# Performance work log

Measured on AMD Instinct MI355X. Metric: run time of the kernel, lower is better.

Reference implementation:

```python
import jax, jax.numpy as jnp
import numpy as np

N_M, N_U = 50000, 100000          # movie / user node counts
D_IN, H, OUT = 128, 128, 64        # input feat, hidden_channels, out_channels
E_SIMS, E_REV = 800000, 1600000    # edge counts


def setup_inputs() -> dict:
    key = jax.random.key(0)
    ks = jax.random.split(key, 16)
    glorot = lambda k, i, o: jax.random.normal(k, (i, o), jnp.float32) * np.float32(1.0 / np.sqrt(i))
    return dict(
        x_movie=jax.random.normal(ks[0], (N_M, D_IN), jnp.float32),
        x_user=jax.random.normal(ks[1], (N_U, D_IN), jnp.float32),
        src_sims=jax.random.randint(ks[2], (E_SIMS,), 0, N_M, jnp.int32),
        dst_sims=jax.random.randint(ks[3], (E_SIMS,), 0, N_M, jnp.int32),
        src_rev=jax.random.randint(ks[4], (E_REV,), 0, N_M, jnp.int32),
        dst_rev=jax.random.randint(ks[5], (E_REV,), 0, N_U, jnp.int32),
        # SAGEConv params: lin_l (neighbor, with bias), lin_r (root, no bias)
        W1l=glorot(ks[6], D_IN, H), b1l=jnp.zeros((H,), jnp.float32), W1r=glorot(ks[7], D_IN, H),
        W2l=glorot(ks[8], D_IN, H), b2l=jnp.zeros((H,), jnp.float32), W2r=glorot(ks[9], D_IN, H),
        W3l=glorot(ks[10], H, H),   b3l=jnp.zeros((H,), jnp.float32), W3r=glorot(ks[11], H, H),
        # Post-conv dense layers
        Wl1=glorot(ks[12], H, H),  bl1=jnp.zeros((H,), jnp.float32),
        Wl2=glorot(ks[13], H, H),  bl2=jnp.zeros((H,), jnp.float32),
        Wl3=glorot(ks[14], H, OUT), bl3=jnp.zeros((OUT,), jnp.float32),
    )


def _sage(x_src, x_dst, src, dst, Wl, bl, Wr):
    """PyG SAGEConv (mean aggr): lin_l(mean_{j->i} x_src[j]) + lin_r(x_dst)."""
    n_dst = x_dst.shape[0]
    summ = jax.ops.segment_sum(x_src[src], dst, num_segments=n_dst)          # [n_dst, d]
    cnt = jax.ops.segment_sum(jnp.ones(src.shape, x_src.dtype), dst, num_segments=n_dst)
    mean = summ / jnp.maximum(cnt, 1.0)[:, None]                             # 0 for isolated nodes
    return mean @ Wl + bl + x_dst @ Wr


def reference(x_movie, x_user, src_sims, dst_sims, src_rev, dst_rev,
              W1l, b1l, W1r, W2l, b2l, W2r, W3l, b3l, W3r,
              Wl1, bl1, Wl2, bl2, Wl3, bl3):
    h = jax.nn.relu(_sage(x_movie, x_movie, src_sims, dst_sims, W1l, b1l, W1r))
    h = jax.nn.relu(h @ Wl1 + bl1)
    u = jax.nn.relu(_sage(x_movie, x_user, src_rev, dst_rev, W2l, b2l, W2r))
    u = jax.nn.relu(u @ Wl2 + bl2)
    u = jax.nn.relu(_sage(h, u, src_rev, dst_rev, W3l, b3l, W3r))
    return u @ Wl3 + bl3                                                     # [N_U, OUT]
```

## Files before the change

### kernel.cpp

```cpp
#include <hip/hip_runtime.h>


typedef float f32x4 __attribute__((ext_vector_type(4)));
typedef __bf16 bf16x8 __attribute__((ext_vector_type(8)));
typedef unsigned short us8 __attribute__((ext_vector_type(8)));
typedef unsigned long long ull;

#define CAP 64

struct BinInit { int off[16]; };

__device__ __forceinline__ unsigned short bf16_rne(float x) {
    unsigned u = __builtin_bit_cast(unsigned, x);
    unsigned r = (u + 0x7fffu + ((u >> 16) & 1u)) >> 16;
    return (unsigned short)r;
}
__device__ __forceinline__ float bf16_to_f(unsigned short b) {
    unsigned u = ((unsigned)b) << 16;
    return __builtin_bit_cast(float, u);
}
__device__ __forceinline__ void split_bf16(float x, unsigned short& h, unsigned short& l) {
    h = bf16_rne(x);
    l = bf16_rne(x - bf16_to_f(h));
}

__global__ __launch_bounds__(256) void prepconv_kernel(
    const float* __restrict__ W1l, const float* __restrict__ W1r,
    const float* __restrict__ W2l, const float* __restrict__ W2r,
    const float* __restrict__ W3l, const float* __restrict__ W3r,
    const float* __restrict__ Wl1, const float* __restrict__ Wl2,
    const float* __restrict__ Wl3,
    unsigned short* __restrict__ oh, unsigned short* __restrict__ ol,
    const float* __restrict__ xm, unsigned short* __restrict__ xmh,
    unsigned short* __restrict__ xml, unsigned short* __restrict__ itab,
    int n8, BinInit bi, int* __restrict__ binoff, int* __restrict__ bin_wcur)
{
    const int t = threadIdx.x;
    if (blockIdx.x == 0 && t < 16) {
        binoff[t] = bi.off[t];
        bin_wcur[t] = bi.off[t];
    }
    if (blockIdx.x < 544) {
        const int i = blockIdx.x * 256 + t;
        float v; int k, n, N, base;
        if (i < 98304) {
            const int s = i >> 15;
            const float* Wa = s == 0 ? W1l : (s == 1 ? W2l : W3l);
            const float* Wb = s == 0 ? W1r : (s == 1 ? W2r : W3r);
            base = s << 15; N = 128;
            const int local = i - base;
            k = local >> 7; n = local & 127;
            v = (k < 128) ? Wa[(size_t)k * 128 + n] : Wb[(size_t)(k - 128) * 128 + n];
        } else if (i < 131072) {
            const int s = (i - 98304) >> 14;
            const float* Wa = s ? Wl2 : Wl1;
            base = 98304 + (s << 14); N = 128;
            const int local = i - base;
            k = local >> 7; n = local & 127;
            v = Wa[(size_t)k * 128 + n];
        } else {
            base = 131072; N = 64;
            const int local = i - base;
            k = local >> 6; n = local & 63;
            v = Wl3[(size_t)k * 64 + n];
        }
        unsigned short h, l;
        split_bf16(v, h, l);
        const int ks = k >> 5, kg = (k >> 3) & 3, j = k & 7;
        const int slot = (n >> 4) * 64 + kg * 16 + (n & 15);
        const size_t pos = (size_t)base + ((size_t)ks * (N * 4) + slot) * 8 + j;
        oh[pos] = h;
        ol[pos] = l;
    } else {
        const int i = (blockIdx.x - 544) * 256 + t;
        if (i >= n8) return;
        us8 hv, lv;
#pragma unroll
        for (int j = 0; j < 8; ++j) {
            const float x = xm[(size_t)i * 8 + j];
            unsigned short h, l;
            split_bf16(x, h, l);
            hv[j] = h; lv[j] = l;
        }
        *(us8*)(xmh + (size_t)i * 8) = hv;
        *(us8*)(xml + (size_t)i * 8) = lv;
        const int r = i >> 4, c = (i & 15) * 8;
        *(us8*)(itab + (size_t)r * 256 + c) = hv;
    }
}

__global__ __launch_bounds__(256) void passA_kernel(
    const int* __restrict__ src_s, const int* __restrict__ dst_s,
    const int* __restrict__ src_r, const int* __restrict__ dst_r,
    int* __restrict__ bin_wcur, unsigned* __restrict__ pairs,
    int ES, int ER, int sm, int su)
{
    __shared__ int lcnt[16], loff[16], lbase[16];
    __shared__ ull stg[2048];
    const int t = threadIdx.x;
    const int total = ES + ER;
    const int base = blockIdx.x * 2048;
    if (t < 16) lcnt[t] = 0;
    __syncthreads();
    int mybin[8], myrank[8];
    ull mypack[8];
#pragma unroll
    for (int e = 0; e < 8; ++e) {
        const int i = base + e * 256 + t;
        mybin[e] = -1;
        if (i < total) {
            int s, d, b, local;
            if (i < ES) { s = src_s[i]; d = dst_s[i]; b = d >> sm; local = d & ((1 << sm) - 1); }
            else { s = src_r[i - ES]; d = dst_r[i - ES]; b = 8 + (d >> su); local = d & ((1 << su) - 1); }
            mybin[e] = b;
            mypack[e] = ((ull)b << 32) | ((unsigned)(local << 16) | (unsigned)s);
            myrank[e] = atomicAdd(&lcnt[b], 1);
        }
    }
    __syncthreads();
    if (t < 16) {
        const int v = lcnt[t];
        int incl = v;
#pragma unroll
        for (int off = 1; off < 16; off <<= 1) {
            const int y = __shfl_up(incl, off, 64);
            if (t >= off) incl += y;
        }
        loff[t] = incl - v;
        lbase[t] = atomicAdd(&bin_wcur[t], v);
    }
    __syncthreads();
#pragma unroll
    for (int e = 0; e < 8; ++e)
        if (mybin[e] >= 0) stg[loff[mybin[e]] + myrank[e]] = mypack[e];
    __syncthreads();
    const int cnt_total = loff[15] + lcnt[15];
    for (int i = t; i < cnt_total; i += 256) {
        const ull p = stg[i];
        const int b = (int)(p >> 32);
        pairs[lbase[b] + (i - loff[b])] = (unsigned)p;
    }
}

__global__ __launch_bounds__(256) void fillB_kernel(
    const unsigned* __restrict__ pairs, const int* __restrict__ binoff,
    const int* __restrict__ bin_wcur,
    int* __restrict__ cnt_m, int* __restrict__ cnt_u,
    int* __restrict__ srcs_s, int* __restrict__ srcs_r, int sm, int su)
{
    const int t = threadIdx.x;
    const int g = blockIdx.x & 7, bi = blockIdx.x >> 3, nb = gridDim.x >> 3;
#pragma unroll
    for (int which = 0; which < 2; ++which) {
        const int b = g + which * 8;
        const int beg = binoff[b], cnt = bin_wcur[b] - beg;
        const int dbase = which ? (g << su) : (g << sm);
        int* __restrict__ cn = which ? cnt_u : cnt_m;
        int* __restrict__ srcs = which ? srcs_r : srcs_s;
        for (int i = bi * 256 + t; i < cnt; i += nb * 256) {
            const unsigned p = pairs[beg + i];
            const int d = (int)(p >> 16) + dbase;
            const int pos = atomicAdd(&cn[d], 1);
            srcs[(size_t)d * CAP + pos] = (int)(p & 0xffffu);
        }
    }
}

__global__ __launch_bounds__(256) void gather_m_kernel(
    const unsigned short* __restrict__ it,
    const int* __restrict__ cnt, const int* __restrict__ srcs,
    unsigned short* __restrict__ o0h, unsigned short* __restrict__ o0l, int n_dst)
{
    const int wid = (blockIdx.x * 256 + threadIdx.x) >> 6;
    const int lane = threadIdx.x & 63;
    if (wid >= n_dst) return;
    const int nE = __builtin_amdgcn_readfirstlane(cnt[wid]);
    const int beg = wid * CAP;
    const int loff = lane * 2;
    float a0 = 0.f, a1 = 0.f;
    int e = 0;
    for (; e + 8 <= nE; e += 8) {
#pragma unroll
        for (int u = 0; u < 8; ++u) {
            const int s = srcs[beg + e + u];
            const unsigned v = *(const unsigned*)(it + (size_t)s * 256 + loff);
            a0 += __builtin_bit_cast(float, v << 16);
            a1 += __builtin_bit_cast(float, v & 0xffff0000u);
        }
    }
    for (; e < nE; ++e) {
        const int s = srcs[beg + e];
        const unsigned v = *(const unsigned*)(it + (size_t)s * 256 + loff);
        a0 += __builtin_bit_cast(float, v << 16);
        a1 += __builtin_bit_cast(float, v & 0xffff0000u);
    }
    const float inv = 1.0f / fmaxf((float)nE, 1.0f);
    unsigned short h0, l0, h1, l1;
    split_bf16(a0 * inv, h0, l0); split_bf16(a1 * inv, h1, l1);
    *(unsigned*)(o0h + (size_t)wid * 128 + loff) = (unsigned)h0 | ((unsigned)h1 << 16);
    *(unsigned*)(o0l + (size_t)wid * 128 + loff) = (unsigned)l0 | ((unsigned)l1 << 16);
}

__global__ __launch_bounds__(256) void gather_u_kernel(
    const unsigned short* __restrict__ it,
    const int* __restrict__ cnt, const int* __restrict__ srcs,
    unsigned short* __restrict__ o0h, unsigned short* __restrict__ o0l,
    unsigned short* __restrict__ o1h, unsigned short* __restrict__ o1l, int n_dst)
{
    const int wid = (blockIdx.x * 256 + threadIdx.x) >> 6;
    const int lane = threadIdx.x & 63;
    if (wid >= n_dst) return;
    const int nE = __builtin_amdgcn_readfirstlane(cnt[wid]);
    const int beg = wid * CAP;
    const int loff = lane * 4;
    float a0 = 0.f, a1 = 0.f, a2 = 0.f, a3 = 0.f;
    int e = 0;
    for (; e + 8 <= nE; e += 8) {
#pragma unroll
        for (int u = 0; u < 8; ++u) {
            const int s = srcs[beg + e + u];
            const uint2 v = *(const uint2*)(it + (size_t)s * 256 + loff);
            a0 += __builtin_bit_cast(float, v.x << 16);
            a1 += __builtin_bit_cast(float, v.x & 0xffff0000u);
            a2 += __builtin_bit_cast(float, v.y << 16);
            a3 += __builtin_bit_cast(float, v.y & 0xffff0000u);
        }
    }
    for (; e < nE; ++e) {
        const int s = srcs[beg + e];
        const uint2 v = *(const uint2*)(it + (size_t)s * 256 + loff);
        a0 += __builtin_bit_cast(float, v.x << 16);
        a1 += __builtin_bit_cast(float, v.x & 0xffff0000u);
        a2 += __builtin_bit_cast(float, v.y << 16);
        a3 += __builtin_bit_cast(float, v.y & 0xffff0000u);
    }
    const float inv = 1.0f / fmaxf((float)nE, 1.0f);
    unsigned short h0, l0, h1, l1, h2, l2, h3, l3;
    split_bf16(a0 * inv, h0, l0); split_bf16(a1 * inv, h1, l1);
    split_bf16(a2 * inv, h2, l2); split_bf16(a3 * inv, h3, l3);
    uint2 hv, lv;
    hv.x = (unsigned)h0 | ((unsigned)h1 << 16);
    hv.y = (unsigned)h2 | ((unsigned)h3 << 16);
    lv.x = (unsigned)l0 | ((unsigned)l1 << 16);
    lv.y = (unsigned)l2 | ((unsigned)l3 << 16);
    if (lane < 32) {
        *(uint2*)(o0h + (size_t)wid * 128 + loff) = hv;
        *(uint2*)(o0l + (size_t)wid * 128 + loff) = lv;
    } else {
        const int c = (lane - 32) * 4;
        *(uint2*)(o1h + (size_t)wid * 128 + c) = hv;
        *(uint2*)(o1l + (size_t)wid * 128 + c) = lv;
    }
}

#define MFMA3(ACC, AH, AL, BH, BL) \
    ACC = __builtin_amdgcn_mfma_f32_16x16x32_bf16( \
        __builtin_bit_cast(bf16x8, AH), __builtin_bit_cast(bf16x8, BH), ACC, 0, 0, 0); \
    ACC = __builtin_amdgcn_mfma_f32_16x16x32_bf16( \
        __builtin_bit_cast(bf16x8, AH), __builtin_bit_cast(bf16x8, BL), ACC, 0, 0, 0); \
    ACC = __builtin_amdgcn_mfma_f32_16x16x32_bf16( \
        __builtin_bit_cast(bf16x8, AL), __builtin_bit_cast(bf16x8, BH), ACC, 0, 0, 0);

__global__ __launch_bounds__(256) void fusedM_kernel(
    const unsigned short* __restrict__ m1h, const unsigned short* __restrict__ m1l,
    const unsigned short* __restrict__ xmh, const unsigned short* __restrict__ xml,
    const unsigned short* __restrict__ w1h, const unsigned short* __restrict__ w1l,
    const float* __restrict__ b1,
    const unsigned short* __restrict__ d1h, const unsigned short* __restrict__ d1l,
    const float* __restrict__ bd1,
    unsigned short* __restrict__ itab, int n)
{
    __shared__ __attribute__((aligned(16))) unsigned short TS[2][128][136];
    const int t = threadIdx.x, lane = t & 63, wv = t >> 6;
    const int wm = wv >> 1, wn = wv & 1;
    const int row0 = blockIdx.x * 128;
    const int r15 = lane & 15, l4 = lane >> 4;
    int arow[4]; bool ainb[4];
#pragma unroll
    for (int m = 0; m < 4; ++m) { arow[m] = row0 + (wm * 4 + m) * 16 + r15; ainb[m] = arow[m] < n; }

    f32x4 acc[4][4];
#pragma unroll
    for (int m = 0; m < 4; ++m)
#pragma unroll
        for (int j = 0; j < 4; ++j) acc[m][j] = (f32x4)0.0f;
#pragma unroll
    for (int ks = 0; ks < 8; ++ks) {
        const bool p1 = ks >= 4;
        const int kf = (ks & 3) * 32 + 8 * l4;
        const unsigned short* __restrict__ ph = p1 ? xmh : m1h;
        const unsigned short* __restrict__ pl = p1 ? xml : m1l;
        us8 ah[4], al[4];
#pragma unroll
        for (int m = 0; m < 4; ++m) {
            ah[m] = ainb[m] ? *(const us8*)(ph + (size_t)arow[m] * 128 + kf) : (us8)(unsigned short)0;
            al[m] = ainb[m] ? *(const us8*)(pl + (size_t)arow[m] * 128 + kf) : (us8)(unsigned short)0;
        }
        us8 bh[4], bl[4];
#pragma unroll
        for (int j = 0; j < 4; ++j) {
            const size_t boff = ((size_t)ks * 512 + (size_t)(wn * 4 + j) * 64 + lane) * 8;
            bh[j] = *(const us8*)(w1h + boff);
            bl[j] = *(const us8*)(w1l + boff);
        }
#pragma unroll
        for (int m = 0; m < 4; ++m)
#pragma unroll
            for (int j = 0; j < 4; ++j) { MFMA3(acc[m][j], ah[m], al[m], bh[j], bl[j]); }
    }
#pragma unroll
    for (int j = 0; j < 4; ++j) {
        const int col = (wn * 4 + j) * 16 + r15;
        const float b = b1[col];
#pragma unroll
        for (int m = 0; m < 4; ++m) {
            const int lrb = (wm * 4 + m) * 16 + l4 * 4;
#pragma unroll
            for (int reg = 0; reg < 4; ++reg) {
                unsigned short h, l;
                split_bf16(fmaxf(acc[m][j][reg] + b, 0.0f), h, l);
                TS[0][lrb + reg][col] = h;
                TS[1][lrb + reg][col] = l;
            }
        }
    }
    __syncthreads();

    f32x4 acc2[4][4];
#pragma unroll
    for (int m = 0; m < 4; ++m)
#pragma unroll
        for (int j = 0; j < 4; ++j) acc2[m][j] = (f32x4)0.0f;
#pragma unroll
    for (int ks = 0; ks < 4; ++ks) {
        const int kf = ks * 32 + 8 * l4;
        us8 ah[4], al[4];
#pragma unroll
        for (int m = 0; m < 4; ++m) {
            const int lr = (wm * 4 + m) * 16 + r15;
            ah[m] = *(const us8*)&TS[0][lr][kf];
            al[m] = *(const us8*)&TS[1][lr][kf];
        }
        us8 bh[4], bl[4];
#pragma unroll
        for (int j = 0; j < 4; ++j) {
            const size_t boff = ((size_t)ks * 512 + (size_t)(wn * 4 + j) * 64 + lane) * 8;
            bh[j] = *(const us8*)(d1h + boff);
            bl[j] = *(const us8*)(d1l + boff);
        }
#pragma unroll
        for (int m = 0; m < 4; ++m)
#pragma unroll
            for (int j = 0; j < 4; ++j) { MFMA3(acc2[m][j], ah[m], al[m], bh[j], bl[j]); }
    }
    __syncthreads();
#pragma unroll
    for (int j = 0; j < 4; ++j) {
        const int col = (wn * 4 + j) * 16 + r15;
        const float b = bd1[col];
#pragma unroll
        for (int m = 0; m < 4; ++m) {
            const int lrb = (wm * 4 + m) * 16 + l4 * 4;
#pragma unroll
            for (int reg = 0; reg < 4; ++reg)
                TS[0][lrb + reg][col] = bf16_rne(fmaxf(acc2[m][j][reg] + b, 0.0f));
        }
    }
    __syncthreads();
#pragma unroll
    for (int ii = 0; ii < 8; ++ii) {
        const int i = t + ii * 256;
        const int r = i >> 4, c = (i & 15) * 8;
        const int grow = row0 + r;
        if (grow < n)
            *(us8*)(itab + (size_t)grow * 256 + 128 + c) = *(const us8*)&TS[0][r][c];
    }
}

__global__ __launch_bounds__(256) void fusedU_kernel(
    const unsigned short* __restrict__ m2h, const unsigned short* __restrict__ m2l,
    const unsigned short* __restrict__ m3h, const unsigned short* __restrict__ m3l,
    const float* __restrict__ xu,
    const unsigned short* __restrict__ w2h, const unsigned short* __restrict__ w2l,
    const float* __restrict__ b2,
    const unsigned short* __restrict__ d2h, const unsigned short* __restrict__ d2l,
    const float* __restrict__ bd2,
    const unsigned short* __restrict__ w3h, const unsigned short* __restrict__ w3l,
    const float* __restrict__ b3,
    const unsigned short* __restrict__ d3h, const unsigned short* __restrict__ d3l,
    const float* __restrict__ bd3,
    float* __restrict__ out, int n)
{
    __shared__ __attribute__((aligned(16))) unsigned short TS[2][128][136];
    const int t = threadIdx.x, lane = t & 63, wv = t >> 6;
    const int wm = wv >> 1, wn = wv & 1;
    const int row0 = blockIdx.x * 128;
    const int r15 = lane & 15, l4 = lane >> 4;
    int arow[4]; bool ainb[4];
#pragma unroll
    for (int m = 0; m < 4; ++m) { arow[m] = row0 + (wm * 4 + m) * 16 + r15; ainb[m] = arow[m] < n; }

    {
        f32x4 acc[4][4];
#pragma unroll
        for (int m = 0; m < 4; ++m)
#pragma unroll
            for (int j = 0; j < 4; ++j) acc[m][j] = (f32x4)0.0f;
#pragma unroll
        for (int ks = 0; ks < 8; ++ks) {
            const bool p1 = ks >= 4;
            const int kf = (ks & 3) * 32 + 8 * l4;
            us8 ah[4], al[4];
            if (!p1) {
#pragma unroll
                for (int m = 0; m < 4; ++m) {
                    ah[m] = ainb[m] ? *(const us8*)(m2h + (size_t)arow[m] * 128 + kf) : (us8)(unsigned short)0;
                    al[m] = ainb[m] ? *(const us8*)(m2l + (size_t)arow[m] * 128 + kf) : (us8)(unsigned short)0;
                }
            } else {
#pragma unroll
                for (int m = 0; m < 4; ++m) {
                    us8 hv = (us8)(unsigned short)0, lv = (us8)(unsigned short)0;
                    if (ainb[m]) {
                        const float* p = xu + (size_t)arow[m] * 128 + kf;
                        const f32x4 v0 = *(const f32x4*)p;
                        const f32x4 v1 = *(const f32x4*)(p + 4);
#pragma unroll
                        for (int jj = 0; jj < 4; ++jj) {
                            unsigned short h, l;
                            split_bf16(v0[jj], h, l); hv[jj] = h; lv[jj] = l;
                        }
#pragma unroll
                        for (int jj = 0; jj < 4; ++jj) {
                            unsigned short h, l;
                            split_bf16(v1[jj], h, l); hv[4 + jj] = h; lv[4 + jj] = l;
                        }
                    }
                    ah[m] = hv; al[m] = lv;
                }
            }
            us8 bh[4], bl[4];
#pragma unroll
            for (int j = 0; j < 4; ++j) {
                const size_t boff = ((size_t)ks * 512 + (size_t)(wn * 4 + j) * 64 + lane) * 8;
                bh[j] = *(const us8*)(w2h + boff);
                bl[j] = *(const us8*)(w2l + boff);
            }
#pragma unroll
            for (int m = 0; m < 4; ++m)
#pragma unroll
                for (int j = 0; j < 4; ++j) { MFMA3(acc[m][j], ah[m], al[m], bh[j], bl[j]); }
        }
#pragma unroll
        for (int j = 0; j < 4; ++j) {
            const int col = (wn * 4 + j) * 16 + r15;
            const float b = b2[col];
#pragma unroll
            for (int m = 0; m < 4; ++m) {
                const int lrb = (wm * 4 + m) * 16 + l4 * 4;
#pragma unroll
                for (int reg = 0; reg < 4; ++reg) {
                    unsigned short h, l;
                    split_bf16(fmaxf(acc[m][j][reg] + b, 0.0f), h, l);
                    TS[0][lrb + reg][col] = h;
                    TS[1][lrb + reg][col] = l;
                }
            }
        }
    }
    __syncthreads();

    {
        f32x4 acc[4][4];
#pragma unroll
        for (int m = 0; m < 4; ++m)
#pragma unroll
            for (int j = 0; j < 4; ++j) acc[m][j] = (f32x4)0.0f;
#pragma unroll
        for (int ks = 0; ks < 4; ++ks) {
            const int kf = ks * 32 + 8 * l4;
            us8 ah[4], al[4];
#pragma unroll
            for (int m = 0; m < 4; ++m) {
                const int lr = (wm * 4 + m) * 16 + r15;
                ah[m] = *(const us8*)&TS[0][lr][kf];
                al[m] = *(const us8*)&TS[1][lr][kf];
            }
            us8 bh[4], bl[4];
#pragma unroll
            for (int j = 0; j < 4; ++j) {
                const size_t boff = ((size_t)ks * 512 + (size_t)(wn * 4 + j) * 64 + lane) * 8;
                bh[j] = *(const us8*)(d2h + boff);
                bl[j] = *(const us8*)(d2l + boff);
            }
#pragma unroll
            for (int m = 0; m < 4; ++m)
#pragma unroll
                for (int j = 0; j < 4; ++j) { MFMA3(acc[m][j], ah[m], al[m], bh[j], bl[j]); }
        }
        __syncthreads();
#pragma unroll
        for (int j = 0; j < 4; ++j) {
            const int col = (wn * 4 + j) * 16 + r15;
            const float b = bd2[col];
#pragma unroll
            for (int m = 0; m < 4; ++m) {
                const int lrb = (wm * 4 + m) * 16 + l4 * 4;
#pragma unroll
                for (int reg = 0; reg < 4; ++reg) {
                    unsigned short h, l;
                    split_bf16(fmaxf(acc[m][j][reg] + b, 0.0f), h, l);
                    TS[0][lrb + reg][col] = h;
                    TS[1][lrb + reg][col] = l;
                }
            }
        }
    }
    __syncthreads();

    {
        f32x4 acc[4][4];
#pragma unroll
        for (int m = 0; m < 4; ++m)
#pragma unroll
            for (int j = 0; j < 4; ++j) acc[m][j] = (f32x4)0.0f;
#pragma unroll
        for (int ks = 0; ks < 8; ++ks) {
            const bool p1 = ks >= 4;
            const int kf = (ks & 3) * 32 + 8 * l4;
            us8 ah[4], al[4];
            if (!p1) {
#pragma unroll
                for (int m = 0; m < 4; ++m) {
                    ah[m] = ainb[m] ? *(const us8*)(m3h + (size_t)arow[m] * 128 + kf) : (us8)(unsigned short)0;
                    al[m] = ainb[m] ? *(const us8*)(m3l + (size_t)arow[m] * 128 + kf) : (us8)(unsigned short)0;
                }
            } else {
#pragma unroll
                for (int m = 0; m < 4; ++m) {
                    const int lr = (wm * 4 + m) * 16 + r15;
                    ah[m] = *(const us8*)&TS[0][lr][kf];
                    al[m] = *(const us8*)&TS[1][lr][kf];
                }
            }
            us8 bh[4], bl[4];
#pragma unroll
            for (int j = 0; j < 4; ++j) {
                const size_t boff = ((size_t)ks * 512 + (size_t)(wn * 4 + j) * 64 + lane) * 8;
                bh[j] = *(const us8*)(w3h + boff);
                bl[j] = *(const us8*)(w3l + boff);
            }
#pragma unroll
            for (int m = 0; m < 4; ++m)
#pragma unroll
                for (int j = 0; j < 4; ++j) { MFMA3(acc[m][j], ah[m], al[m], bh[j], bl[j]); }
        }
        __syncthreads();
#pragma unroll
        for (int j = 0; j < 4; ++j) {
            const int col = (wn * 4 + j) * 16 + r15;
            const float b = b3[col];
#pragma unroll
            for (int m = 0; m < 4; ++m) {
                const int lrb = (wm * 4 + m) * 16 + l4 * 4;
#pragma unroll
                for (int reg = 0; reg < 4; ++reg) {
                    unsigned short h, l;
                    split_bf16(fmaxf(acc[m][j][reg] + b, 0.0f), h, l);
                    TS[0][lrb + reg][col] = h;
                    TS[1][lrb + reg][col] = l;
                }
            }
        }
    }
    __syncthreads();

    {
        f32x4 acc[4][2];
#pragma unroll
        for (int m = 0; m < 4; ++m)
#pragma unroll
            for (int j = 0; j < 2; ++j) acc[m][j] = (f32x4)0.0f;
#pragma unroll
        for (int ks = 0; ks < 4; ++ks) {
            const int kf = ks * 32 + 8 * l4;
            us8 ah[4], al[4];
#pragma unroll
            for (int m = 0; m < 4; ++m) {
                const int lr = (wm * 4 + m) * 16 + r15;
                ah[m] = *(const us8*)&TS[0][lr][kf];
                al[m] = *(const us8*)&TS[1][lr][kf];
            }
            us8 bh[2], bl[2];
#pragma unroll
            for (int j = 0; j < 2; ++j) {
                const size_t boff = ((size_t)ks * 256 + (size_t)(wn * 2 + j) * 64 + lane) * 8;
                bh[j] = *(const us8*)(d3h + boff);
                bl[j] = *(const us8*)(d3l + boff);
            }
#pragma unroll
            for (int m = 0; m < 4; ++m)
#pragma unroll
                for (int j = 0; j < 2; ++j) { MFMA3(acc[m][j], ah[m], al[m], bh[j], bl[j]); }
        }
        __syncthreads();
        float (*F)[68] = (float(*)[68])&TS[0][0][0];
#pragma unroll
        for (int j = 0; j < 2; ++j) {
            const int col = (wn * 2 + j) * 16 + r15;
            const float b = bd3[col];
#pragma unroll
            for (int m = 0; m < 4; ++m) {
                const int lrb = (wm * 4 + m) * 16 + l4 * 4;
#pragma unroll
                for (int reg = 0; reg < 4; ++reg)
                    F[lrb + reg][col] = acc[m][j][reg] + b;
            }
        }
        __syncthreads();
#pragma unroll
        for (int ii = 0; ii < 8; ++ii) {
            const int i = t + ii * 256;
            const int r = i >> 4, c = (i & 15) * 4;
            const int grow = row0 + r;
            if (grow < n)
                *(f32x4*)(out + (size_t)grow * 64 + c) = *(const f32x4*)&F[r][c];
        }
    }
}

extern "C" void kernel_launch(void* const* d_in, const int* in_sizes, int n_in,
                              void* d_out, int out_size, void* d_ws, size_t ws_size,
                              hipStream_t stream) {
    const float* x_movie = (const float*)d_in[0];
    const float* x_user  = (const float*)d_in[1];
    const int* src_sims  = (const int*)d_in[2];
    const int* dst_sims  = (const int*)d_in[3];
    const int* src_rev   = (const int*)d_in[4];
    const int* dst_rev   = (const int*)d_in[5];
    const float* W1l = (const float*)d_in[6];
    const float* b1l = (const float*)d_in[7];
    const float* W1r = (const float*)d_in[8];
    const float* W2l = (const float*)d_in[9];
    const float* b2l = (const float*)d_in[10];
    const float* W2r = (const float*)d_in[11];
    const float* W3l = (const float*)d_in[12];
    const float* b3l = (const float*)d_in[13];
    const float* W3r = (const float*)d_in[14];
    const float* Wl1 = (const float*)d_in[15];
    const float* bl1 = (const float*)d_in[16];
    const float* Wl2 = (const float*)d_in[17];
    const float* bl2 = (const float*)d_in[18];
    const float* Wl3 = (const float*)d_in[19];
    const float* bl3 = (const float*)d_in[20];
    float* out = (float*)d_out;

    const int NM = in_sizes[0] / 128;
    const int NU = in_sizes[1] / 128;
    const int ES = in_sizes[2];
    const int ER = in_sizes[4];

    int sm = 0; while (((NM - 1) >> sm) > 7) sm++;
    int su = 0; while (((NU - 1) >> su) > 7) su++;

    BinInit bi;
    {
        long cum = 0;
        for (int b = 0; b < 8; ++b) {
            bi.off[b] = (int)cum;
            long lo = (long)b << sm;
            long span = (long)NM - lo;
            if (span < 0) span = 0;
            if (span > (1L << sm)) span = 1L << sm;
            long cap = span > 0 ? (long)((double)ES * span / NM) + 16384 : 0;
            cum += cap;
        }
        for (int b = 0; b < 8; ++b) {
            bi.off[8 + b] = (int)cum;
            long lo = (long)b << su;
            long span = (long)NU - lo;
            if (span < 0) span = 0;
            if (span > (1L << su)) span = 1L << su;
            long cap = span > 0 ? (long)((double)ER * span / NU) + 16384 : 0;
            cum += cap;
        }
    }

    const size_t SZ_M = (size_t)NM * 128;
    const size_t SZ_U = (size_t)NU * 128;

    unsigned short* us = (unsigned short*)d_ws;
    size_t o = 0;
    unsigned short* itab = us + o; o += 2 * SZ_M;
    unsigned short* xmh = us + o; o += SZ_M;
    unsigned short* xml = us + o; o += SZ_M;
    unsigned short* m1h = us + o; o += SZ_M;
    unsigned short* m1l = us + o; o += SZ_M;
    unsigned short* m2h = us + o; o += SZ_U;
    unsigned short* m2l = us + o; o += SZ_U;
    unsigned short* m3h = us + o; o += SZ_U;
    unsigned short* m3l = us + o; o += SZ_U;
    unsigned short* whi = us + o; o += 139264;
    unsigned short* wlo = us + o; o += 139264;
    int* ip = (int*)(us + o);
    int* cnt_m    = ip;
    int* cnt_u    = cnt_m + NM;
    int* binoff   = cnt_u + NU;
    int* bin_wcur = binoff + 16;
    int* srcs_sims = bin_wcur + 16;
    int* srcs_rev  = srcs_sims + (size_t)NM * CAP;

    unsigned* pairs = (unsigned*)m2h;

    const int W1O = 0, W2O = 32768, W3O = 65536, D1O = 98304, D2O = 114688, D3O = 131072;

    const dim3 blk(256);
    const int gM = (NM + 127) / 128;
    const int gU = (NU + 127) / 128;
    const int nA  = (ES + ER + 2047) / 2048;
    const int nConv = (NM * 16 + 255) / 256;

    hipMemsetAsync(cnt_m, 0, (size_t)(NM + NU) * sizeof(int), stream);
    prepconv_kernel<<<544 + nConv, blk, 0, stream>>>(
        W1l, W1r, W2l, W2r, W3l, W3r, Wl1, Wl2, Wl3, whi, wlo,
        x_movie, xmh, xml, itab, NM * 16, bi, binoff, bin_wcur);
    passA_kernel<<<nA, blk, 0, stream>>>(src_sims, dst_sims, src_rev, dst_rev,
                                         bin_wcur, pairs, ES, ER, sm, su);
    fillB_kernel<<<1024, blk, 0, stream>>>(pairs, binoff, bin_wcur,
                                           cnt_m, cnt_u, srcs_sims, srcs_rev, sm, su);

    gather_m_kernel<<<(NM + 3) / 4, blk, 0, stream>>>(
        itab, cnt_m, srcs_sims, m1h, m1l, NM);
    fusedM_kernel<<<gM, blk, 0, stream>>>(
        m1h, m1l, xmh, xml, whi + W1O, wlo + W1O, b1l,
        whi + D1O, wlo + D1O, bl1, itab, NM);
    gather_u_kernel<<<(NU + 3) / 4, blk, 0, stream>>>(
        itab, cnt_u, srcs_rev, m2h, m2l, m3h, m3l, NU);
    fusedU_kernel<<<gU, blk, 0, stream>>>(
        m2h, m2l, m3h, m3l, x_user,
        whi + W2O, wlo + W2O, b2l, whi + D2O, wlo + D2O, bl2,
        whi + W3O, wlo + W3O, b3l, whi + D3O, wlo + D3O, bl3,
        out, NU);
}
```

Before: 431.2 us.

## Split interleaved gather table and regroup gathers into two independent passes

Replaces the interleaved 256-wide table (x_movie hi | h) with separate 128-wide tables. The x_movie gathers for both the sims and rev edges run in one combined kernel before fusedM, and the h gather for users runs afterwards. The rev edge list is now walked twice, each time at half row width, instead of once at full width. The goal is to drop the interleaved table copy and balance the gather work, at the cost of extra index reads and of touching each x_movie row in a separate pass.

```diff
diff --git a/kernel.cpp b/kernel.cpp
--- a/kernel.cpp
+++ b/kernel.cpp
@@ -32,7 +32,7 @@
     const float* __restrict__ Wl3,
     unsigned short* __restrict__ oh, unsigned short* __restrict__ ol,
     const float* __restrict__ xm, unsigned short* __restrict__ xmh,
-    unsigned short* __restrict__ xml, unsigned short* __restrict__ itab,
+    unsigned short* __restrict__ xml,
     int n8, BinInit bi, int* __restrict__ binoff, int* __restrict__ bin_wcur)
 {
     const int t = threadIdx.x;
@@ -84,8 +84,6 @@
         }
         *(us8*)(xmh + (size_t)i * 8) = hv;
         *(us8*)(xml + (size_t)i * 8) = lv;
-        const int r = i >> 4, c = (i & 15) * 8;
-        *(us8*)(itab + (size_t)r * 256 + c) = hv;
     }
 }
 
@@ -166,8 +164,51 @@
     }
 }
 
-__global__ __launch_bounds__(256) void gather_m_kernel(
-    const unsigned short* __restrict__ it,
+__global__ __launch_bounds__(256) void gatherA_kernel(
+    const unsigned short* __restrict__ tab,
+    const int* __restrict__ cnt_m, const int* __restrict__ srcs_m,
+    const int* __restrict__ cnt_u, const int* __restrict__ srcs_u,
+    unsigned short* __restrict__ m1h, unsigned short* __restrict__ m1l,
+    unsigned short* __restrict__ m2h, unsigned short* __restrict__ m2l,
+    int NM, int NU)
+{
+    const int wid = (blockIdx.x * 256 + threadIdx.x) >> 6;
+    const int lane = threadIdx.x & 63;
+    if (wid >= NM + NU) return;
+    const bool isu = wid >= NM;
+    const int d = isu ? wid - NM : wid;
+    const int nE = __builtin_amdgcn_readfirstlane(isu ? cnt_u[d] : cnt_m[d]);
+    const int* __restrict__ srcs = isu ? srcs_u : srcs_m;
+    const int beg = d * CAP;
+    const int loff = lane * 2;
+    float a0 = 0.f, a1 = 0.f;
+    int e = 0;
+    for (; e + 8 <= nE; e += 8) {
+#pragma unroll
+        for (int u = 0; u < 8; ++u) {
+            const int s = srcs[beg + e + u];
+            const unsigned v = *(const unsigned*)(tab + (size_t)s * 128 + loff);
+            a0 += __builtin_bit_cast(float, v << 16);
+            a1 += __builtin_bit_cast(float, v & 0xffff0000u);
+        }
+    }
+    for (; e < nE; ++e) {
+        const int s = srcs[beg + e];
+        const unsigned v = *(const unsigned*)(tab + (size_t)s * 128 + loff);
+        a0 += __builtin_bit_cast(float, v << 16);
+        a1 += __builtin_bit_cast(float, v & 0xffff0000u);
+    }
+    const float inv = 1.0f / fmaxf((float)nE, 1.0f);
+    unsigned short h0, l0, h1, l1;
+    split_bf16(a0 * inv, h0, l0); split_bf16(a1 * inv, h1, l1);
+    unsigned short* __restrict__ oh = isu ? m2h : m1h;
+    unsigned short* __restrict__ ol = isu ? m2l : m1l;
+    *(unsigned*)(oh + (size_t)d * 128 + loff) = (unsigned)h0 | ((unsigned)h1 << 16);
+    *(unsigned*)(ol + (size_t)d * 128 + loff) = (unsigned)l0 | ((unsigned)l1 << 16);
+}
+
+__global__ __launch_bounds__(256) void gatherB_kernel(
+    const unsigned short* __restrict__ tab,
     const int* __restrict__ cnt, const int* __restrict__ srcs,
     unsigned short* __restrict__ o0h, unsigned short* __restrict__ o0l, int n_dst)
 {
@@ -183,14 +224,14 @@
 #pragma unroll
         for (int u = 0; u < 8; ++u) {
             const int s = srcs[beg + e + u];
-            const unsigned v = *(const unsigned*)(it + (size_t)s * 256 + loff);
+            const unsigned v = *(const unsigned*)(tab + (size_t)s * 128 + loff);
             a0 += __builtin_bit_cast(float, v << 16);
             a1 += __builtin_bit_cast(float, v & 0xffff0000u);
         }
     }
     for (; e < nE; ++e) {
         const int s = srcs[beg + e];
-        const unsigned v = *(const unsigned*)(it + (size_t)s * 256 + loff);
+        const unsigned v = *(const unsigned*)(tab + (size_t)s * 128 + loff);
         a0 += __builtin_bit_cast(float, v << 16);
         a1 += __builtin_bit_cast(float, v & 0xffff0000u);
     }
@@ -199,58 +240,6 @@
     split_bf16(a0 * inv, h0, l0); split_bf16(a1 * inv, h1, l1);
     *(unsigned*)(o0h + (size_t)wid * 128 + loff) = (unsigned)h0 | ((unsigned)h1 << 16);
     *(unsigned*)(o0l + (size_t)wid * 128 + loff) = (unsigned)l0 | ((unsigned)l1 << 16);
-}
-
-__global__ __launch_bounds__(256) void gather_u_kernel(
-    const unsigned short* __restrict__ it,
-    const int* __restrict__ cnt, const int* __restrict__ srcs,
-    unsigned short* __restrict__ o0h, unsigned short* __restrict__ o0l,
-    unsigned short* __restrict__ o1h, unsigned short* __restrict__ o1l, int n_dst)
-{
-    const int wid = (blockIdx.x * 256 + threadIdx.x) >> 6;
-    const int lane = threadIdx.x & 63;
-    if (wid >= n_dst) return;
-    const int nE = __builtin_amdgcn_readfirstlane(cnt[wid]);
-    const int beg = wid * CAP;
-    const int loff = lane * 4;
-    float a0 = 0.f, a1 = 0.f, a2 = 0.f, a3 = 0.f;
-    int e = 0;
-    for (; e + 8 <= nE; e += 8) {
-#pragma unroll
-        for (int u = 0; u < 8; ++u) {
-            const int s = srcs[beg + e + u];
-            const uint2 v = *(const uint2*)(it + (size_t)s * 256 + loff);
-            a0 += __builtin_bit_cast(float, v.x << 16);
-            a1 += __builtin_bit_cast(float, v.x & 0xffff0000u);
-            a2 += __builtin_bit_cast(float, v.y << 16);
-            a3 += __builtin_bit_cast(float, v.y & 0xffff0000u);
-        }
-    }
-    for (; e < nE; ++e) {
-        const int s = srcs[beg + e];
-        const uint2 v = *(const uint2*)(it + (size_t)s * 256 + loff);
-        a0 += __builtin_bit_cast(float, v.x << 16);
-        a1 += __builtin_bit_cast(float, v.x & 0xffff0000u);
-        a2 += __builtin_bit_cast(float, v.y << 16);
-        a3 += __builtin_bit_cast(float, v.y & 0xffff0000u);
-    }
-    const float inv = 1.0f / fmaxf((float)nE, 1.0f);
-    unsigned short h0, l0, h1, l1, h2, l2, h3, l3;
-    split_bf16(a0 * inv, h0, l0); split_bf16(a1 * inv, h1, l1);
-    split_bf16(a2 * inv, h2, l2); split_bf16(a3 * inv, h3, l3);
-    uint2 hv, lv;
-    hv.x = (unsigned)h0 | ((unsigned)h1 << 16);
-    hv.y = (unsigned)h2 | ((unsigned)h3 << 16);
-    lv.x = (unsigned)l0 | ((unsigned)l1 << 16);
-    lv.y = (unsigned)l2 | ((unsigned)l3 << 16);
-    if (lane < 32) {
-        *(uint2*)(o0h + (size_t)wid * 128 + loff) = hv;
-        *(uint2*)(o0l + (size_t)wid * 128 + loff) = lv;
-    } else {
-        const int c = (lane - 32) * 4;
-        *(uint2*)(o1h + (size_t)wid * 128 + c) = hv;
-        *(uint2*)(o1l + (size_t)wid * 128 + c) = lv;
-    }
 }
 
 #define MFMA3(ACC, AH, AL, BH, BL) \
@@ -268,7 +257,7 @@
     const float* __restrict__ b1,
     const unsigned short* __restrict__ d1h, const unsigned short* __restrict__ d1l,
     const float* __restrict__ bd1,
-    unsigned short* __restrict__ itab, int n)
+    unsigned short* __restrict__ h_s, int n)
 {
     __shared__ __attribute__((aligned(16))) unsigned short TS[2][128][136];
     const int t = threadIdx.x, lane = t & 63, wv = t >> 6;
@@ -373,7 +362,7 @@
         const int r = i >> 4, c = (i & 15) * 8;
         const int grow = row0 + r;
         if (grow < n)
-            *(us8*)(itab + (size_t)grow * 256 + 128 + c) = *(const us8*)&TS[0][r][c];
+            *(us8*)(h_s + (size_t)grow * 128 + c) = *(const us8*)&TS[0][r][c];
     }
 }
 
@@ -691,9 +680,9 @@
 
     unsigned short* us = (unsigned short*)d_ws;
     size_t o = 0;
-    unsigned short* itab = us + o; o += 2 * SZ_M;
     unsigned short* xmh = us + o; o += SZ_M;
     unsigned short* xml = us + o; o += SZ_M;
+    unsigned short* h_s = us + o; o += SZ_M;
     unsigned short* m1h = us + o; o += SZ_M;
     unsigned short* m1l = us + o; o += SZ_M;
     unsigned short* m2h = us + o; o += SZ_U;
@@ -723,19 +712,19 @@
     hipMemsetAsync(cnt_m, 0, (size_t)(NM + NU) * sizeof(int), stream);
     prepconv_kernel<<<544 + nConv, blk, 0, stream>>>(
         W1l, W1r, W2l, W2r, W3l, W3r, Wl1, Wl2, Wl3, whi, wlo,
-        x_movie, xmh, xml, itab, NM * 16, bi, binoff, bin_wcur);
+        x_movie, xmh, xml, NM * 16, bi, binoff, bin_wcur);
     passA_kernel<<<nA, blk, 0, stream>>>(src_sims, dst_sims, src_rev, dst_rev,
                                          bin_wcur, pairs, ES, ER, sm, su);
     fillB_kernel<<<1024, blk, 0, stream>>>(pairs, binoff, bin_wcur,
                                            cnt_m, cnt_u, srcs_sims, srcs_rev, sm, su);
 
-    gather_m_kernel<<<(NM + 3) / 4, blk, 0, stream>>>(
-        itab, cnt_m, srcs_sims, m1h, m1l, NM);
+    gatherA_kernel<<<(NM + NU + 3) / 4, blk, 0, stream>>>(
+        xmh, cnt_m, srcs_sims, cnt_u, srcs_rev, m1h, m1l, m2h, m2l, NM, NU);
     fusedM_kernel<<<gM, blk, 0, stream>>>(
         m1h, m1l, xmh, xml, whi + W1O, wlo + W1O, b1l,
-        whi + D1O, wlo + D1O, bl1, itab, NM);
-    gather_u_kernel<<<(NU + 3) / 4, blk, 0, stream>>>(
-        itab, cnt_u, srcs_rev, m2h, m2l, m3h, m3l, NU);
+        whi + D1O, wlo + D1O, bl1, h_s, NM);
+    gatherB_kernel<<<(NU + 3) / 4, blk, 0, stream>>>(
+        h_s, cnt_u, srcs_rev, m3h, m3l, NU);
     fusedU_kernel<<<gU, blk, 0, stream>>>(
         m2h, m2l, m3h, m3l, x_user,
         whi + W2O, wlo + W2O, b2l, whi + D2O, wlo + D2O, bl2,
```

Result: slower. 452.8 us (+5.0%).
